# Optimization experiments

Measured on AMD Instinct MI355X. Metric: run time of the kernel, lower is better.

The kernel has to match this reference:

```python
import jax, jax.numpy as jnp
import numpy as np

N = 50000      # nodes
E = 200000     # edges
IN = 768       # in_dim
HID = 256      # hidden_dim
OUT = 64       # out_dim
H = 4          # heads in conv1
R = 6          # n_relations
NEG = 0.2      # LeakyReLU negative slope (PyG default)
EPS = 1e-5     # LayerNorm eps


def layer_norm(h, g, b):
    mu = jnp.mean(h, axis=-1, keepdims=True)
    var = jnp.mean((h - mu) ** 2, axis=-1, keepdims=True)
    return (h - mu) * jax.lax.rsqrt(var + EPS) * g + b


def gat_layer(x, src, dst, W, a_src, a_dst, bias, heads, dh):
    # project: [N, heads, dh]
    h = (x @ W).reshape(-1, heads, dh)
    # per-node attention logits [N, heads]
    al_s = jnp.sum(h * a_src, axis=-1)
    al_d = jnp.sum(h * a_dst, axis=-1)
    # per-edge scores (edge j->i: source contributes al_s[j], target al_d[i])
    e = jax.nn.leaky_relu(al_s[src] + al_d[dst], NEG)  # [E, heads]
    # segment softmax over edges sharing the same destination node
    e_max = jax.ops.segment_max(e, dst, num_segments=N)        # [N, heads]
    ex = jnp.exp(e - e_max[dst])                               # [E, heads]
    denom = jax.ops.segment_sum(ex, dst, num_segments=N)       # [N, heads]
    alpha = ex / denom[dst]                                    # [E, heads]
    # weighted scatter-aggregate of source messages
    msg = h[src] * alpha[:, :, None]                            # [E, heads, dh]
    out = jax.ops.segment_sum(msg, dst, num_segments=N)        # [N, heads, dh]
    return out.reshape(-1, heads * dh) + bias


def setup_inputs() -> dict:
    key = jax.random.key(0)
    ks = jax.random.split(key, 16)
    s = 0.05  # keep attention logits tame
    return {
        "x": jax.random.normal(ks[0], (N, IN), jnp.float32),
        "edge_index": jax.random.randint(ks[1], (2, E), 0, N, dtype=jnp.int64),
        "edge_type": jax.random.randint(ks[2], (E,), 0, R, dtype=jnp.int64),
        "edge_emb": jax.random.normal(ks[3], (R, IN), jnp.float32) * s,
        "W1": jax.random.normal(ks[4], (IN, H * (HID // H)), jnp.float32) * s,
        "a_src1": jax.random.normal(ks[5], (H, HID // H), jnp.float32) * s,
        "a_dst1": jax.random.normal(ks[6], (H, HID // H), jnp.float32) * s,
        "b1": jnp.zeros((HID,), jnp.float32),
        "g1": jnp.ones((HID,), jnp.float32),
        "be1": jnp.zeros((HID,), jnp.float32),
        "W2": jax.random.normal(ks[7], (HID, OUT), jnp.float32) * s,
        "a_src2": jax.random.normal(ks[8], (1, OUT), jnp.float32) * s,
        "a_dst2": jax.random.normal(ks[9], (1, OUT), jnp.float32) * s,
        "b2": jnp.zeros((OUT,), jnp.float32),
        "g2": jnp.ones((OUT,), jnp.float32),
        "be2": jnp.zeros((OUT,), jnp.float32),
    }


def reference(x, edge_index, edge_type, edge_emb, W1, a_src1, a_dst1, b1, g1, be1,
              W2, a_src2, a_dst2, b2, g2, be2):
    src, dst = edge_index[0], edge_index[1]
    edge_feat = edge_emb[edge_type]                 # [E, IN]
    x_mod = x.at[src].set(x[src] + edge_feat)
    h = gat_layer(x_mod, src, dst, W1, a_src1, a_dst1, b1, H, HID // H)
    h = layer_norm(h, g1, be1)
    h = jax.nn.elu(h)                                # dropout off (inference)
    h = gat_layer(h, src, dst, W2, a_src2, a_dst2, b2, 1, OUT)
    h = layer_norm(h, g2, be2)
    return h
```

## Files before the change

kernel.cpp:

```cpp
#include <hip/hip_runtime.h>
#include <cstdint>
#include <cstddef>

#define NN 50000
#define NE 200000
#define IND 768
#define HID 256
#define OUTD 64
#define NB 196

typedef __bf16 bf16;
typedef __bf16 bf16x8 __attribute__((ext_vector_type(8)));
typedef float f32x4 __attribute__((ext_vector_type(4)));

__global__ __launch_bounds__(256) void k_edge_prep(const int* __restrict__ ei,
                                                   int* __restrict__ le, int* __restrict__ deg) {
  int e = blockIdx.x * 256 + threadIdx.x;
  if (e < NE) {
    atomicMax(&le[ei[e]], e);
    atomicAdd(&deg[ei[NE + e]], 1);
  }
}

__global__ __launch_bounds__(256) void k_scan_block(const int* __restrict__ deg,
                                                    int* __restrict__ excl, int* __restrict__ bsum) {
  __shared__ int sm[256];
  int tid = threadIdx.x;
  int i = blockIdx.x * 256 + tid;
  int v = (i < NN) ? deg[i] : 0;
  sm[tid] = v;
  __syncthreads();
#pragma unroll
  for (int off = 1; off < 256; off <<= 1) {
    int t = (tid >= off) ? sm[tid - off] : 0;
    __syncthreads();
    sm[tid] += t;
    __syncthreads();
  }
  if (i < NN) excl[i] = sm[tid] - v;
  if (tid == 255) bsum[blockIdx.x] = sm[255];
}

__global__ __launch_bounds__(256) void k_scan_partials(const int* __restrict__ bsum,
                                                       int* __restrict__ bbase) {
  __shared__ int sm[256];
  int tid = threadIdx.x;
  int v = (tid < NB) ? bsum[tid] : 0;
  sm[tid] = v;
  __syncthreads();
#pragma unroll
  for (int off = 1; off < 256; off <<= 1) {
    int t = (tid >= off) ? sm[tid - off] : 0;
    __syncthreads();
    sm[tid] += t;
    __syncthreads();
  }
  bbase[tid] = sm[tid] - v;
}

__global__ __launch_bounds__(256) void k_add_base(const int* __restrict__ excl,
                                                  const int* __restrict__ bbase,
                                                  int* __restrict__ rowstart, int* __restrict__ cur) {
  int i = blockIdx.x * 256 + threadIdx.x;
  if (i < NN) {
    int rs = excl[i] + bbase[i >> 8];
    rowstart[i] = rs;
    cur[i] = rs;
  }
}

__global__ __launch_bounds__(256) void k_scatter_csr(const int* __restrict__ ei,
                                                     int* __restrict__ cur, int* __restrict__ csr) {
  int e = blockIdx.x * 256 + threadIdx.x;
  if (e < NE) {
    int d = ei[NE + e];
    int pos = atomicAdd(&cur[d], 1);
    csr[pos] = ei[e];
  }
}

__global__ __launch_bounds__(256) void k_transpose(const float* __restrict__ W,
                                                   bf16* __restrict__ Wt, int K, int NC) {
  int k = blockIdx.x * 256 + threadIdx.x;
  int n = blockIdx.y;
  if (k < K) Wt[n * K + k] = (bf16)W[k * NC + n];
}

template <typename OutT, bool FUSE>
__global__ __launch_bounds__(256) void k_gemm_bt(const bf16* __restrict__ A,
                                                 const float* __restrict__ Ax,
                                                 const int* __restrict__ le,
                                                 const int* __restrict__ et,
                                                 const float* __restrict__ eemb,
                                                 const bf16* __restrict__ Bt,
                                                 OutT* __restrict__ C,
                                                 int M, int K, int NC,
                                                 const float* __restrict__ aS,
                                                 const float* __restrict__ aD,
                                                 float* __restrict__ alS,
                                                 float* __restrict__ alD,
                                                 int alStride) {
  __shared__ bf16 As[128 * 32];
  __shared__ bf16 Bs[128 * 32];
  const int tid = threadIdx.x;
  const int lane = tid & 63;
  const int wave = tid >> 6;
  const int wr = wave >> 1, wc = wave & 1;
  const int ln15 = lane & 15, q = lane >> 4;
  const int n0 = blockIdx.x * 128;
  const int m0 = blockIdx.y * 128;
  const int r0 = tid >> 2;
  const int ce = (tid & 3) << 3;

  const int rA1 = min(m0 + r0, M - 1);
  const int rA2 = min(m0 + 64 + r0, M - 1);
  const int rB1 = min(n0 + r0, NC - 1);
  const int rB2 = min(n0 + 64 + r0, NC - 1);

  int e1 = -1, e2 = -1;
  if (FUSE) {
    int l1 = le[rA1]; if (l1 >= 0) e1 = et[l1];
    int l2 = le[rA2]; if (l2 >= 0) e2 = et[l2];
  }

  f32x4 acc[4][4] = {};

  for (int kt = 0; kt < K; kt += 32) {
    bf16x8 va, vb;
    int4 va_i, vb_i;
    if (FUSE) {
      const float* p1 = Ax + (size_t)rA1 * K + kt + ce;
      const float* p2 = Ax + (size_t)rA2 * K + kt + ce;
      float4 a0 = *(const float4*)p1, a1 = *(const float4*)(p1 + 4);
      float4 b0 = *(const float4*)p2, b1 = *(const float4*)(p2 + 4);
      if (e1 >= 0) {
        const float* q1 = eemb + (size_t)e1 * K + kt + ce;
        float4 t0 = *(const float4*)q1, t1 = *(const float4*)(q1 + 4);
        a0.x += t0.x; a0.y += t0.y; a0.z += t0.z; a0.w += t0.w;
        a1.x += t1.x; a1.y += t1.y; a1.z += t1.z; a1.w += t1.w;
      }
      if (e2 >= 0) {
        const float* q2 = eemb + (size_t)e2 * K + kt + ce;
        float4 t0 = *(const float4*)q2, t1 = *(const float4*)(q2 + 4);
        b0.x += t0.x; b0.y += t0.y; b0.z += t0.z; b0.w += t0.w;
        b1.x += t1.x; b1.y += t1.y; b1.z += t1.z; b1.w += t1.w;
      }
      va[0] = (bf16)a0.x; va[1] = (bf16)a0.y; va[2] = (bf16)a0.z; va[3] = (bf16)a0.w;
      va[4] = (bf16)a1.x; va[5] = (bf16)a1.y; va[6] = (bf16)a1.z; va[7] = (bf16)a1.w;
      vb[0] = (bf16)b0.x; vb[1] = (bf16)b0.y; vb[2] = (bf16)b0.z; vb[3] = (bf16)b0.w;
      vb[4] = (bf16)b1.x; vb[5] = (bf16)b1.y; vb[6] = (bf16)b1.z; vb[7] = (bf16)b1.w;
    } else {
      va_i = *(const int4*)(A + (size_t)rA1 * K + kt + ce);
      vb_i = *(const int4*)(A + (size_t)rA2 * K + kt + ce);
    }
    int4 wb1 = *(const int4*)(Bt + (size_t)rB1 * K + kt + ce);
    int4 wb2 = *(const int4*)(Bt + (size_t)rB2 * K + kt + ce);
    __syncthreads();
    if (FUSE) {
      *(bf16x8*)(As + r0 * 32 + ce) = va;
      *(bf16x8*)(As + (64 + r0) * 32 + ce) = vb;
    } else {
      *(int4*)(As + r0 * 32 + ce) = va_i;
      *(int4*)(As + (64 + r0) * 32 + ce) = vb_i;
    }
    *(int4*)(Bs + r0 * 32 + ce) = wb1;
    *(int4*)(Bs + (64 + r0) * 32 + ce) = wb2;
    __syncthreads();
    bf16x8 af[4], bfr[4];
#pragma unroll
    for (int i = 0; i < 4; i++)
      af[i] = *(const bf16x8*)(As + (wr * 64 + i * 16 + ln15) * 32 + q * 8);
#pragma unroll
    for (int i = 0; i < 4; i++)
      bfr[i] = *(const bf16x8*)(Bs + (wc * 64 + i * 16 + ln15) * 32 + q * 8);
#pragma unroll
    for (int mi = 0; mi < 4; mi++)
#pragma unroll
      for (int ni = 0; ni < 4; ni++)
        acc[mi][ni] = __builtin_amdgcn_mfma_f32_16x16x32_bf16(af[mi], bfr[ni], acc[mi][ni], 0, 0, 0);
  }

#pragma unroll
  for (int mi = 0; mi < 4; mi++)
#pragma unroll
    for (int ni = 0; ni < 4; ni++)
#pragma unroll
      for (int r = 0; r < 4; r++) {
        int row = m0 + wr * 64 + mi * 16 + q * 4 + r;
        int col = n0 + wc * 64 + ni * 16 + ln15;
        if (row < M && col < NC) C[(size_t)row * NC + col] = (OutT)acc[mi][ni][r];
      }

  if (n0 + wc * 64 < NC) {
    const int hd = (n0 + wc * 64) >> 6;
#pragma unroll
    for (int mi = 0; mi < 4; mi++)
#pragma unroll
      for (int r = 0; r < 4; r++) {
        float ps = 0.f, pd = 0.f;
#pragma unroll
        for (int ni = 0; ni < 4; ni++) {
          int col = n0 + wc * 64 + ni * 16 + ln15;
          float w_s = (col < NC) ? aS[col] : 0.f;
          float w_d = (col < NC) ? aD[col] : 0.f;
          ps += acc[mi][ni][r] * w_s;
          pd += acc[mi][ni][r] * w_d;
        }
#pragma unroll
        for (int off = 1; off < 16; off <<= 1) {
          ps += __shfl_xor(ps, off);
          pd += __shfl_xor(pd, off);
        }
        int row = m0 + wr * 64 + mi * 16 + q * 4 + r;
        if (ln15 == 0 && row < M) {
          alS[row * alStride + hd] = ps;
          alD[row * alStride + hd] = pd;
        }
      }
  }
}

__global__ __launch_bounds__(256) void k_agg_ln1(const int* __restrict__ rowstart,
                                                 const int* __restrict__ deg,
                                                 const int* __restrict__ csr,
                                                 const bf16* __restrict__ h1,
                                                 const float* __restrict__ alS,
                                                 const float* __restrict__ alD,
                                                 const float* __restrict__ b1,
                                                 const float* __restrict__ g1,
                                                 const float* __restrict__ be1,
                                                 bf16* __restrict__ hln) {
  __shared__ float red[8];
  int n = blockIdx.x, f = threadIdx.x, hd = f >> 6;
  int start = rowstart[n], cnt = deg[n];
  float ald = alD[n * 4 + hd];
  float accv = 0.f, accw = 0.f;
  for (int j = 0; j < cnt; j++) {
    int s = csr[start + j];
    float logit = alS[s * 4 + hd] + ald;
    logit = logit >= 0.f ? logit : 0.2f * logit;
    float w = __expf(logit);
    accv += w * (float)h1[(size_t)s * HID + f];
    accw += w;
  }
  float v = (cnt > 0) ? accv / accw : 0.f;
  v += b1[f];
  float s = v, ss = v * v;
#pragma unroll
  for (int off = 32; off; off >>= 1) { s += __shfl_xor(s, off); ss += __shfl_xor(ss, off); }
  if ((f & 63) == 0) { red[f >> 6] = s; red[4 + (f >> 6)] = ss; }
  __syncthreads();
  float tot = red[0] + red[1] + red[2] + red[3];
  float tss = red[4] + red[5] + red[6] + red[7];
  float mu = tot * (1.f / HID);
  float var = tss * (1.f / HID) - mu * mu;
  float y = (v - mu) * rsqrtf(var + 1e-5f) * g1[f] + be1[f];
  y = y > 0.f ? y : __expf(y) - 1.f;
  hln[(size_t)n * HID + f] = (bf16)y;
}

__global__ __launch_bounds__(64) void k_agg_ln2(const int* __restrict__ rowstart,
                                                const int* __restrict__ deg,
                                                const int* __restrict__ csr,
                                                const float* __restrict__ h2,
                                                const float* __restrict__ alS,
                                                const float* __restrict__ alD,
                                                const float* __restrict__ b2,
                                                const float* __restrict__ g2,
                                                const float* __restrict__ be2,
                                                float* __restrict__ out) {
  int n = blockIdx.x, f = threadIdx.x;
  int start = rowstart[n], cnt = deg[n];
  float ald = alD[n];
  float accv = 0.f, accw = 0.f;
  for (int j = 0; j < cnt; j++) {
    int s = csr[start + j];
    float logit = alS[s] + ald;
    logit = logit >= 0.f ? logit : 0.2f * logit;
    float w = __expf(logit);
    accv += w * h2[(size_t)s * OUTD + f];
    accw += w;
  }
  float v = (cnt > 0) ? accv / accw : 0.f;
  v += b2[f];
  float s = v, ss = v * v;
#pragma unroll
  for (int off = 32; off; off >>= 1) { s += __shfl_xor(s, off); ss += __shfl_xor(ss, off); }
  float mu = s * (1.f / OUTD);
  float var = ss * (1.f / OUTD) - mu * mu;
  out[(size_t)n * OUTD + f] = (v - mu) * rsqrtf(var + 1e-5f) * g2[f] + be2[f];
}

extern "C" void kernel_launch(void* const* d_in, const int* in_sizes, int n_in,
                              void* d_out, int out_size, void* d_ws, size_t ws_size,
                              hipStream_t stream) {
  const float* x    = (const float*)d_in[0];
  const int*   ei   = (const int*)d_in[1];
  const int*   et   = (const int*)d_in[2];
  const float* eemb = (const float*)d_in[3];
  const float* W1   = (const float*)d_in[4];
  const float* as1  = (const float*)d_in[5];
  const float* ad1  = (const float*)d_in[6];
  const float* b1   = (const float*)d_in[7];
  const float* g1   = (const float*)d_in[8];
  const float* be1  = (const float*)d_in[9];
  const float* W2   = (const float*)d_in[10];
  const float* as2  = (const float*)d_in[11];
  const float* ad2  = (const float*)d_in[12];
  const float* b2   = (const float*)d_in[13];
  const float* g2   = (const float*)d_in[14];
  const float* be2  = (const float*)d_in[15];
  float* out = (float*)d_out;

  char* base = (char*)d_ws;
  size_t off = 0;
  auto alloc = [&](size_t bytes) -> void* {
    void* p = base + off;
    off = (off + bytes + 255) & ~(size_t)255;
    return p;
  };
  int*   le    = (int*)alloc((size_t)NN * 4);
  int*   deg   = (int*)alloc((size_t)NN * 4);
  int*   excl  = (int*)alloc((size_t)NN * 4);
  int*   bsum  = (int*)alloc(256 * 4);
  int*   bbase = (int*)alloc(256 * 4);
  int*   rowst = (int*)alloc((size_t)NN * 4);
  int*   cur   = (int*)alloc((size_t)NN * 4);
  int*   csr   = (int*)alloc((size_t)NE * 4);
  bf16*  h1    = (bf16*)alloc((size_t)NN * HID * 2);
  float* alS1  = (float*)alloc((size_t)NN * 4 * 4);
  float* alD1  = (float*)alloc((size_t)NN * 4 * 4);
  bf16*  hln   = (bf16*)alloc((size_t)NN * HID * 2);
  float* h2    = (float*)alloc((size_t)NN * OUTD * 4);
  float* alS2  = (float*)alloc((size_t)NN * 4);
  float* alD2  = (float*)alloc((size_t)NN * 4);
  bf16*  W1t   = (bf16*)alloc((size_t)HID * IND * 2);
  bf16*  W2t   = (bf16*)alloc((size_t)OUTD * HID * 2);

  hipMemsetAsync(le, 0xFF, (size_t)NN * 4, stream);
  hipMemsetAsync(deg, 0, (size_t)NN * 4, stream);

  k_edge_prep<<<(NE + 255) / 256, 256, 0, stream>>>(ei, le, deg);
  k_scan_block<<<NB, 256, 0, stream>>>(deg, excl, bsum);
  k_scan_partials<<<1, 256, 0, stream>>>(bsum, bbase);
  k_add_base<<<NB, 256, 0, stream>>>(excl, bbase, rowst, cur);
  k_scatter_csr<<<(NE + 255) / 256, 256, 0, stream>>>(ei, cur, csr);

  k_transpose<<<dim3(3, HID), 256, 0, stream>>>(W1, W1t, IND, HID);
  k_transpose<<<dim3(1, OUTD), 256, 0, stream>>>(W2, W2t, HID, OUTD);

  k_gemm_bt<bf16, true><<<dim3(2, (NN + 127) / 128), 256, 0, stream>>>(
      nullptr, x, le, et, eemb, W1t, h1, NN, IND, HID, as1, ad1, alS1, alD1, 4);
  k_agg_ln1<<<NN, 256, 0, stream>>>(rowst, deg, csr, h1, alS1, alD1, b1, g1, be1, hln);

  k_gemm_bt<float, false><<<dim3(1, (NN + 127) / 128), 256, 0, stream>>>(
      hln, nullptr, nullptr, nullptr, nullptr, W2t, h2, NN, HID, OUTD, as2, ad2, alS2, alD2, 1);
  k_agg_ln2<<<NN, 64, 0, stream>>>(rowst, deg, csr, h2, alS2, alD2, b2, g2, be2, out);
}
```

Before: 480.0 us.

## Precompute edge-embedding projection, use direct global-to-LDS loads, batch gathers in aggregation

The edge-type embedding is projected through W1 once in a prep kernel (a 6x256 table P) and added in the GEMM epilogue, so the GEMM no longer loads and adds embedding rows per tile. Both GEMMs now stage tiles with global_load_lds into XOR-swizzled shared memory; GEMM1 keeps fp32 A in LDS and converts to bf16 at fragment load. The aggregation kernels unroll the neighbor loop by 8 to issue gathers ahead of use, and layer-2 aggregation packs four nodes per block. Adding P after the bf16 GEMM changes rounding compared with adding the embedding before rounding, and fp32 A in LDS doubles its footprint.

New measurement: 518.4 us. +8.0%, slower.

```diff
diff --git a/kernel.cpp b/kernel.cpp
--- a/kernel.cpp
+++ b/kernel.cpp
@@ -12,6 +12,11 @@
 typedef __bf16 bf16;
 typedef __bf16 bf16x8 __attribute__((ext_vector_type(8)));
 typedef float f32x4 __attribute__((ext_vector_type(4)));
+
+__device__ __forceinline__ void ld_lds16(const void* g, void* l) {
+  __builtin_amdgcn_global_load_lds((const __attribute__((address_space(1))) void*)g,
+                                   (__attribute__((address_space(3))) void*)l, 16, 0, 0);
+}
 
 __global__ __launch_bounds__(256) void k_edge_prep(const int* __restrict__ ei,
                                                    int* __restrict__ le, int* __restrict__ deg) {
@@ -60,12 +65,17 @@
 
 __global__ __launch_bounds__(256) void k_add_base(const int* __restrict__ excl,
                                                   const int* __restrict__ bbase,
-                                                  int* __restrict__ rowstart, int* __restrict__ cur) {
+                                                  const int* __restrict__ le,
+                                                  const int* __restrict__ et,
+                                                  int* __restrict__ rowstart, int* __restrict__ cur,
+                                                  int* __restrict__ tmod) {
   int i = blockIdx.x * 256 + threadIdx.x;
   if (i < NN) {
     int rs = excl[i] + bbase[i >> 8];
     rowstart[i] = rs;
     cur[i] = rs;
+    int l = le[i];
+    tmod[i] = (l >= 0) ? et[l] : -1;
   }
 }
 
@@ -79,100 +89,83 @@
   }
 }
 
-__global__ __launch_bounds__(256) void k_transpose(const float* __restrict__ W,
-                                                   bf16* __restrict__ Wt, int K, int NC) {
-  int k = blockIdx.x * 256 + threadIdx.x;
-  int n = blockIdx.y;
-  if (k < K) Wt[n * K + k] = (bf16)W[k * NC + n];
-}
-
-template <typename OutT, bool FUSE>
-__global__ __launch_bounds__(256) void k_gemm_bt(const bf16* __restrict__ A,
-                                                 const float* __restrict__ Ax,
-                                                 const int* __restrict__ le,
-                                                 const int* __restrict__ et,
-                                                 const float* __restrict__ eemb,
-                                                 const bf16* __restrict__ Bt,
-                                                 OutT* __restrict__ C,
-                                                 int M, int K, int NC,
-                                                 const float* __restrict__ aS,
-                                                 const float* __restrict__ aD,
-                                                 float* __restrict__ alS,
-                                                 float* __restrict__ alD,
-                                                 int alStride) {
-  __shared__ bf16 As[128 * 32];
+__global__ __launch_bounds__(256) void k_prep(const float* __restrict__ W1,
+                                              const float* __restrict__ W2,
+                                              const float* __restrict__ eemb,
+                                              bf16* __restrict__ W1t,
+                                              bf16* __restrict__ W2t,
+                                              float* __restrict__ P) {
+  int b = blockIdx.x, tid = threadIdx.x;
+  if (b < 768) {
+    int k = b, n = tid;
+    W1t[n * 768 + k] = (bf16)W1[k * 256 + n];
+  } else if (b < 768 + 64) {
+    int k = (b - 768) * 4 + (tid >> 6);
+    int n = tid & 63;
+    W2t[n * 256 + k] = (bf16)W2[k * 64 + n];
+  } else {
+    int r = b - 832, c = tid;
+    float s = 0.f;
+    for (int k = 0; k < 768; k++) s += eemb[r * 768 + k] * W1[k * 256 + c];
+    P[r * 256 + c] = s;
+  }
+}
+
+__global__ __launch_bounds__(256) void k_gemm1(const float* __restrict__ Ax,
+                                               const bf16* __restrict__ Bt,
+                                               const int* __restrict__ tmod,
+                                               const float* __restrict__ P,
+                                               bf16* __restrict__ C,
+                                               const float* __restrict__ aS,
+                                               const float* __restrict__ aD,
+                                               float* __restrict__ alS,
+                                               float* __restrict__ alD) {
+  __shared__ float As[128 * 32];
   __shared__ bf16 Bs[128 * 32];
-  const int tid = threadIdx.x;
-  const int lane = tid & 63;
-  const int wave = tid >> 6;
+  const int tid = threadIdx.x, lane = tid & 63, wave = tid >> 6;
   const int wr = wave >> 1, wc = wave & 1;
   const int ln15 = lane & 15, q = lane >> 4;
-  const int n0 = blockIdx.x * 128;
-  const int m0 = blockIdx.y * 128;
-  const int r0 = tid >> 2;
-  const int ce = (tid & 3) << 3;
-
-  const int rA1 = min(m0 + r0, M - 1);
-  const int rA2 = min(m0 + 64 + r0, M - 1);
-  const int rB1 = min(n0 + r0, NC - 1);
-  const int rB2 = min(n0 + 64 + r0, NC - 1);
-
-  int e1 = -1, e2 = -1;
-  if (FUSE) {
-    int l1 = le[rA1]; if (l1 >= 0) e1 = et[l1];
-    int l2 = le[rA2]; if (l2 >= 0) e2 = et[l2];
-  }
+  const int n0 = blockIdx.x * 128, m0 = blockIdx.y * 128;
+
+  const int a_lrow = lane >> 3, a_gch = (lane & 7) ^ a_lrow;
+  const int b_lrow = lane >> 2, b_gch = (lane & 3) ^ ((b_lrow >> 1) & 3);
 
   f32x4 acc[4][4] = {};
 
-  for (int kt = 0; kt < K; kt += 32) {
-    bf16x8 va, vb;
-    int4 va_i, vb_i;
-    if (FUSE) {
-      const float* p1 = Ax + (size_t)rA1 * K + kt + ce;
-      const float* p2 = Ax + (size_t)rA2 * K + kt + ce;
-      float4 a0 = *(const float4*)p1, a1 = *(const float4*)(p1 + 4);
-      float4 b0 = *(const float4*)p2, b1 = *(const float4*)(p2 + 4);
-      if (e1 >= 0) {
-        const float* q1 = eemb + (size_t)e1 * K + kt + ce;
-        float4 t0 = *(const float4*)q1, t1 = *(const float4*)(q1 + 4);
-        a0.x += t0.x; a0.y += t0.y; a0.z += t0.z; a0.w += t0.w;
-        a1.x += t1.x; a1.y += t1.y; a1.z += t1.z; a1.w += t1.w;
-      }
-      if (e2 >= 0) {
-        const float* q2 = eemb + (size_t)e2 * K + kt + ce;
-        float4 t0 = *(const float4*)q2, t1 = *(const float4*)(q2 + 4);
-        b0.x += t0.x; b0.y += t0.y; b0.z += t0.z; b0.w += t0.w;
-        b1.x += t1.x; b1.y += t1.y; b1.z += t1.z; b1.w += t1.w;
-      }
-      va[0] = (bf16)a0.x; va[1] = (bf16)a0.y; va[2] = (bf16)a0.z; va[3] = (bf16)a0.w;
-      va[4] = (bf16)a1.x; va[5] = (bf16)a1.y; va[6] = (bf16)a1.z; va[7] = (bf16)a1.w;
-      vb[0] = (bf16)b0.x; vb[1] = (bf16)b0.y; vb[2] = (bf16)b0.z; vb[3] = (bf16)b0.w;
-      vb[4] = (bf16)b1.x; vb[5] = (bf16)b1.y; vb[6] = (bf16)b1.z; vb[7] = (bf16)b1.w;
-    } else {
-      va_i = *(const int4*)(A + (size_t)rA1 * K + kt + ce);
-      vb_i = *(const int4*)(A + (size_t)rA2 * K + kt + ce);
-    }
-    int4 wb1 = *(const int4*)(Bt + (size_t)rB1 * K + kt + ce);
-    int4 wb2 = *(const int4*)(Bt + (size_t)rB2 * K + kt + ce);
-    __syncthreads();
-    if (FUSE) {
-      *(bf16x8*)(As + r0 * 32 + ce) = va;
-      *(bf16x8*)(As + (64 + r0) * 32 + ce) = vb;
-    } else {
-      *(int4*)(As + r0 * 32 + ce) = va_i;
-      *(int4*)(As + (64 + r0) * 32 + ce) = vb_i;
-    }
-    *(int4*)(Bs + r0 * 32 + ce) = wb1;
-    *(int4*)(Bs + (64 + r0) * 32 + ce) = wb2;
-    __syncthreads();
+  for (int kt = 0; kt < IND; kt += 32) {
+    __syncthreads();
+#pragma unroll
+    for (int j = 0; j < 4; j++) {
+      int g = wave * 4 + j;
+      int grow = min(m0 + g * 8 + a_lrow, NN - 1);
+      ld_lds16(Ax + (size_t)grow * IND + kt + a_gch * 4, As + g * 256);
+    }
+#pragma unroll
+    for (int j = 0; j < 2; j++) {
+      int h = wave * 2 + j;
+      int grow = h * 16 + b_lrow;
+      ld_lds16(Bt + (size_t)(n0 + grow) * IND + kt + b_gch * 8, Bs + h * 512);
+    }
+    __syncthreads();
+
     bf16x8 af[4], bfr[4];
-#pragma unroll
-    for (int i = 0; i < 4; i++)
-      af[i] = *(const bf16x8*)(As + (wr * 64 + i * 16 + ln15) * 32 + q * 8);
-#pragma unroll
-    for (int i = 0; i < 4; i++)
-      bfr[i] = *(const bf16x8*)(Bs + (wc * 64 + i * 16 + ln15) * 32 + q * 8);
+    const float4* Asv = (const float4*)As;
+#pragma unroll
+    for (int mi = 0; mi < 4; mi++) {
+      int R = wr * 64 + mi * 16 + ln15, msk = R & 7;
+      float4 f0 = Asv[R * 8 + ((2 * q) ^ msk)];
+      float4 f1 = Asv[R * 8 + ((2 * q + 1) ^ msk)];
+      bf16x8 t;
+      t[0] = (bf16)f0.x; t[1] = (bf16)f0.y; t[2] = (bf16)f0.z; t[3] = (bf16)f0.w;
+      t[4] = (bf16)f1.x; t[5] = (bf16)f1.y; t[6] = (bf16)f1.z; t[7] = (bf16)f1.w;
+      af[mi] = t;
+    }
+#pragma unroll
+    for (int ni = 0; ni < 4; ni++) {
+      int R = wc * 64 + ni * 16 + ln15;
+      int c = q ^ ((R >> 1) & 3);
+      bfr[ni] = *(const bf16x8*)(Bs + R * 32 + c * 8);
+    }
 #pragma unroll
     for (int mi = 0; mi < 4; mi++)
 #pragma unroll
@@ -180,43 +173,100 @@
         acc[mi][ni] = __builtin_amdgcn_mfma_f32_16x16x32_bf16(af[mi], bfr[ni], acc[mi][ni], 0, 0, 0);
   }
 
-#pragma unroll
-  for (int mi = 0; mi < 4; mi++)
-#pragma unroll
-    for (int ni = 0; ni < 4; ni++)
-#pragma unroll
-      for (int r = 0; r < 4; r++) {
-        int row = m0 + wr * 64 + mi * 16 + q * 4 + r;
+  const int hd = (n0 + wc * 64) >> 6;
+#pragma unroll
+  for (int mi = 0; mi < 4; mi++) {
+#pragma unroll
+    for (int r = 0; r < 4; r++) {
+      int row = m0 + wr * 64 + mi * 16 + q * 4 + r;
+      bool vr = row < NN;
+      int t = tmod[vr ? row : NN - 1];
+      float ps = 0.f, pd = 0.f;
+#pragma unroll
+      for (int ni = 0; ni < 4; ni++) {
         int col = n0 + wc * 64 + ni * 16 + ln15;
-        if (row < M && col < NC) C[(size_t)row * NC + col] = (OutT)acc[mi][ni][r];
+        float val = acc[mi][ni][r];
+        if (t >= 0) val += P[t * HID + col];
+        ps += val * aS[col];
+        pd += val * aD[col];
+        if (vr) C[(size_t)row * HID + col] = (bf16)val;
       }
-
-  if (n0 + wc * 64 < NC) {
-    const int hd = (n0 + wc * 64) >> 6;
-#pragma unroll
-    for (int mi = 0; mi < 4; mi++)
-#pragma unroll
-      for (int r = 0; r < 4; r++) {
-        float ps = 0.f, pd = 0.f;
-#pragma unroll
-        for (int ni = 0; ni < 4; ni++) {
-          int col = n0 + wc * 64 + ni * 16 + ln15;
-          float w_s = (col < NC) ? aS[col] : 0.f;
-          float w_d = (col < NC) ? aD[col] : 0.f;
-          ps += acc[mi][ni][r] * w_s;
-          pd += acc[mi][ni][r] * w_d;
-        }
-#pragma unroll
-        for (int off = 1; off < 16; off <<= 1) {
-          ps += __shfl_xor(ps, off);
-          pd += __shfl_xor(pd, off);
-        }
-        int row = m0 + wr * 64 + mi * 16 + q * 4 + r;
-        if (ln15 == 0 && row < M) {
-          alS[row * alStride + hd] = ps;
-          alD[row * alStride + hd] = pd;
-        }
+#pragma unroll
+      for (int o = 1; o < 16; o <<= 1) { ps += __shfl_xor(ps, o); pd += __shfl_xor(pd, o); }
+      if (ln15 == 0 && vr) { alS[row * 4 + hd] = ps; alD[row * 4 + hd] = pd; }
+    }
+  }
+}
+
+__global__ __launch_bounds__(256) void k_gemm2(const bf16* __restrict__ A,
+                                               const bf16* __restrict__ Bt,
+                                               float* __restrict__ C,
+                                               const float* __restrict__ aS,
+                                               const float* __restrict__ aD,
+                                               float* __restrict__ alS,
+                                               float* __restrict__ alD) {
+  __shared__ bf16 As[128 * 32];
+  __shared__ bf16 Bs[64 * 32];
+  const int tid = threadIdx.x, lane = tid & 63, wave = tid >> 6;
+  const int ln15 = lane & 15, q = lane >> 4;
+  const int m0 = blockIdx.x * 128;
+  const int b_lrow = lane >> 2, b_gch = (lane & 3) ^ ((b_lrow >> 1) & 3);
+
+  f32x4 acc[2][4] = {};
+
+  for (int kt = 0; kt < HID; kt += 32) {
+    __syncthreads();
+#pragma unroll
+    for (int j = 0; j < 2; j++) {
+      int h = wave * 2 + j;
+      int grow = min(m0 + h * 16 + b_lrow, NN - 1);
+      ld_lds16(A + (size_t)grow * HID + kt + b_gch * 8, As + h * 512);
+    }
+    {
+      int grow = wave * 16 + b_lrow;
+      ld_lds16(Bt + (size_t)grow * HID + kt + b_gch * 8, Bs + wave * 512);
+    }
+    __syncthreads();
+
+    bf16x8 af[2], bfr[4];
+#pragma unroll
+    for (int mi = 0; mi < 2; mi++) {
+      int R = wave * 32 + mi * 16 + ln15;
+      int c = q ^ ((R >> 1) & 3);
+      af[mi] = *(const bf16x8*)(As + R * 32 + c * 8);
+    }
+#pragma unroll
+    for (int ni = 0; ni < 4; ni++) {
+      int R = ni * 16 + ln15;
+      int c = q ^ ((R >> 1) & 3);
+      bfr[ni] = *(const bf16x8*)(Bs + R * 32 + c * 8);
+    }
+#pragma unroll
+    for (int mi = 0; mi < 2; mi++)
+#pragma unroll
+      for (int ni = 0; ni < 4; ni++)
+        acc[mi][ni] = __builtin_amdgcn_mfma_f32_16x16x32_bf16(af[mi], bfr[ni], acc[mi][ni], 0, 0, 0);
+  }
+
+#pragma unroll
+  for (int mi = 0; mi < 2; mi++) {
+#pragma unroll
+    for (int r = 0; r < 4; r++) {
+      int row = m0 + wave * 32 + mi * 16 + q * 4 + r;
+      bool vr = row < NN;
+      float ps = 0.f, pd = 0.f;
+#pragma unroll
+      for (int ni = 0; ni < 4; ni++) {
+        int col = ni * 16 + ln15;
+        float val = acc[mi][ni][r];
+        ps += val * aS[col];
+        pd += val * aD[col];
+        if (vr) C[(size_t)row * OUTD + col] = val;
       }
+#pragma unroll
+      for (int o = 1; o < 16; o <<= 1) { ps += __shfl_xor(ps, o); pd += __shfl_xor(pd, o); }
+      if (ln15 == 0 && vr) { alS[row] = ps; alD[row] = pd; }
+    }
   }
 }
 
@@ -235,13 +285,22 @@
   int start = rowstart[n], cnt = deg[n];
   float ald = alD[n * 4 + hd];
   float accv = 0.f, accw = 0.f;
-  for (int j = 0; j < cnt; j++) {
-    int s = csr[start + j];
-    float logit = alS[s * 4 + hd] + ald;
-    logit = logit >= 0.f ? logit : 0.2f * logit;
-    float w = __expf(logit);
-    accv += w * (float)h1[(size_t)s * HID + f];
-    accw += w;
+  for (int j0 = 0; j0 < cnt; j0 += 8) {
+    int m = cnt - j0; m = m > 8 ? 8 : m;
+    int sj[8]; float wv[8];
+#pragma unroll
+    for (int jj = 0; jj < 8; jj++) sj[jj] = (jj < m) ? csr[start + j0 + jj] : 0;
+#pragma unroll
+    for (int jj = 0; jj < 8; jj++) {
+      float lg = alS[sj[jj] * 4 + hd] + ald;
+      lg = lg >= 0.f ? lg : 0.2f * lg;
+      wv[jj] = (jj < m) ? __expf(lg) : 0.f;
+    }
+#pragma unroll
+    for (int jj = 0; jj < 8; jj++) {
+      accv += wv[jj] * (float)h1[(size_t)sj[jj] * HID + f];
+      accw += wv[jj];
+    }
   }
   float v = (cnt > 0) ? accv / accw : 0.f;
   v += b1[f];
@@ -259,27 +318,37 @@
   hln[(size_t)n * HID + f] = (bf16)y;
 }
 
-__global__ __launch_bounds__(64) void k_agg_ln2(const int* __restrict__ rowstart,
-                                                const int* __restrict__ deg,
-                                                const int* __restrict__ csr,
-                                                const float* __restrict__ h2,
-                                                const float* __restrict__ alS,
-                                                const float* __restrict__ alD,
-                                                const float* __restrict__ b2,
-                                                const float* __restrict__ g2,
-                                                const float* __restrict__ be2,
-                                                float* __restrict__ out) {
-  int n = blockIdx.x, f = threadIdx.x;
+__global__ __launch_bounds__(256) void k_agg_ln2(const int* __restrict__ rowstart,
+                                                 const int* __restrict__ deg,
+                                                 const int* __restrict__ csr,
+                                                 const float* __restrict__ h2,
+                                                 const float* __restrict__ alS,
+                                                 const float* __restrict__ alD,
+                                                 const float* __restrict__ b2,
+                                                 const float* __restrict__ g2,
+                                                 const float* __restrict__ be2,
+                                                 float* __restrict__ out) {
+  int n = blockIdx.x * 4 + (threadIdx.x >> 6);
+  int f = threadIdx.x & 63;
   int start = rowstart[n], cnt = deg[n];
   float ald = alD[n];
   float accv = 0.f, accw = 0.f;
-  for (int j = 0; j < cnt; j++) {
-    int s = csr[start + j];
-    float logit = alS[s] + ald;
-    logit = logit >= 0.f ? logit : 0.2f * logit;
-    float w = __expf(logit);
-    accv += w * h2[(size_t)s * OUTD + f];
-    accw += w;
+  for (int j0 = 0; j0 < cnt; j0 += 8) {
+    int m = cnt - j0; m = m > 8 ? 8 : m;
+    int sj[8]; float wv[8];
+#pragma unroll
+    for (int jj = 0; jj < 8; jj++) sj[jj] = (jj < m) ? csr[start + j0 + jj] : 0;
+#pragma unroll
+    for (int jj = 0; jj < 8; jj++) {
+      float lg = alS[sj[jj]] + ald;
+      lg = lg >= 0.f ? lg : 0.2f * lg;
+      wv[jj] = (jj < m) ? __expf(lg) : 0.f;
+    }
+#pragma unroll
+    for (int jj = 0; jj < 8; jj++) {
+      accv += wv[jj] * h2[(size_t)sj[jj] * OUTD + f];
+      accw += wv[jj];
+    }
   }
   float v = (cnt > 0) ? accv / accw : 0.f;
   v += b2[f];
@@ -326,6 +395,7 @@
   int*   bbase = (int*)alloc(256 * 4);
   int*   rowst = (int*)alloc((size_t)NN * 4);
   int*   cur   = (int*)alloc((size_t)NN * 4);
+  int*   tmod  = (int*)alloc((size_t)NN * 4);
   int*   csr   = (int*)alloc((size_t)NE * 4);
   bf16*  h1    = (bf16*)alloc((size_t)NN * HID * 2);
   float* alS1  = (float*)alloc((size_t)NN * 4 * 4);
@@ -336,6 +406,7 @@
   float* alD2  = (float*)alloc((size_t)NN * 4);
   bf16*  W1t   = (bf16*)alloc((size_t)HID * IND * 2);
   bf16*  W2t   = (bf16*)alloc((size_t)OUTD * HID * 2);
+  float* P     = (float*)alloc(6 * HID * 4);
 
   hipMemsetAsync(le, 0xFF, (size_t)NN * 4, stream);
   hipMemsetAsync(deg, 0, (size_t)NN * 4, stream);
@@ -343,17 +414,14 @@
   k_edge_prep<<<(NE + 255) / 256, 256, 0, stream>>>(ei, le, deg);
   k_scan_block<<<NB, 256, 0, stream>>>(deg, excl, bsum);
   k_scan_partials<<<1, 256, 0, stream>>>(bsum, bbase);
-  k_add_base<<<NB, 256, 0, stream>>>(excl, bbase, rowst, cur);
+  k_add_base<<<NB, 256, 0, stream>>>(excl, bbase, le, et, rowst, cur, tmod);
   k_scatter_csr<<<(NE + 255) / 256, 256, 0, stream>>>(ei, cur, csr);
 
-  k_transpose<<<dim3(3, HID), 256, 0, stream>>>(W1, W1t, IND, HID);
-  k_transpose<<<dim3(1, OUTD), 256, 0, stream>>>(W2, W2t, HID, OUTD);
-
-  k_gemm_bt<bf16, true><<<dim3(2, (NN + 127) / 128), 256, 0, stream>>>(
-      nullptr, x, le, et, eemb, W1t, h1, NN, IND, HID, as1, ad1, alS1, alD1, 4);
+  k_prep<<<838, 256, 0, stream>>>(W1, W2, eemb, W1t, W2t, P);
+
+  k_gemm1<<<dim3(2, (NN + 127) / 128), 256, 0, stream>>>(x, W1t, tmod, P, h1, as1, ad1, alS1, alD1);
   k_agg_ln1<<<NN, 256, 0, stream>>>(rowst, deg, csr, h1, alS1, alD1, b1, g1, be1, hln);
 
-  k_gemm_bt<float, false><<<dim3(1, (NN + 127) / 128), 256, 0, stream>>>(
-      hln, nullptr, nullptr, nullptr, nullptr, W2t, h2, NN, HID, OUTD, as2, ad2, alS2, alD2, 1);
-  k_agg_ln2<<<NN, 64, 0, stream>>>(rowst, deg, csr, h2, alS2, alD2, b2, g2, be2, out);
-}
+  k_gemm2<<<(NN + 127) / 128, 256, 0, stream>>>(hln, W2t, h2, as2, ad2, alS2, alD2);
+  k_agg_ln2<<<NN / 4, 256, 0, stream>>>(rowst, deg, csr, h2, alS2, alD2, b2, g2, be2, out);
+}
```
